# Kernel optimization log

Measured on AMD Instinct MI355X. Metric: run time of the kernel, lower is better.

The kernel has to match this reference:

```python
import jax, jax.numpy as jnp
import numpy as np

TEMPERATURE = 0.1
NEG_INF = -1e30


def setup_inputs() -> dict:
    key = jax.random.key(0)
    kf, kl = jax.random.split(key)
    N, D = 8192, 128
    features = jax.random.normal(kf, (N, D), dtype=jnp.float32)
    # labels in [-1, 80): -1 marks background rows that are filtered out
    labels = jax.random.randint(kl, (N,), -1, 80)
    return {"features": features, "labels": labels}


def reference(features, labels):
    N = labels.shape[0]
    fg = labels >= 0  # [N]

    # F.normalize(p=2, dim=1): x / max(||x||, eps)
    norm = jnp.maximum(jnp.linalg.norm(features, axis=1, keepdims=True), 1e-12)
    f = features / norm

    sim = jnp.matmul(f, f.T) / TEMPERATURE  # [N, N]

    pair_fg = fg[:, None] & fg[None, :]
    eye = jnp.eye(N, dtype=bool)
    label_eq = labels[:, None] == labels[None, :]
    pos_mask = pair_fg & label_eq & ~eye          # positives (same label, not self)
    all_mask = pair_fg & ~eye                     # pos | neg == everything but self (within fg)

    # row-wise masked max, clamped to [-20, 20] as in the original
    max_sim = jnp.max(jnp.where(all_mask, sim, NEG_INF), axis=1)
    max_sim = jnp.clip(max_sim, -20.0, 20.0)

    e = jnp.exp(sim - max_sim[:, None])           # cos-sim/temp is bounded, no overflow
    pos_sum = jnp.clip(jnp.sum(jnp.where(pos_mask, e, 0.0), axis=1), 1e-6, 1e6)
    all_sum = jnp.clip(jnp.sum(jnp.where(all_mask, e, 0.0), axis=1), 1e-6, 1e6)

    loss_i = jnp.minimum(-jnp.log(pos_sum / all_sum), 10.0)  # clamp(max=10)

    # rows contributing to the mean: fg rows with at least one positive
    valid = fg & (jnp.sum(pos_mask, axis=1) > 0)
    n_valid = jnp.sum(valid)
    mean_loss = jnp.sum(jnp.where(valid, loss_i, 0.0)) / jnp.maximum(n_valid, 1).astype(jnp.float32)

    ok = (jnp.sum(fg) >= 2) & (n_valid > 0)
    return jnp.where(ok, mean_loss, jnp.float32(0.0))
```

## Files before the change

kernel.cpp:

```cpp
#include <hip/hip_runtime.h>

#define N 8192
#define D 128
#define CHUNK 512
#define NCHUNK (N / CHUNK)
#define TILE_IT (CHUNK / 128)
#define NBIN 81

typedef unsigned short u16;
typedef __attribute__((ext_vector_type(8))) __bf16 bf16x8;
typedef __attribute__((ext_vector_type(4))) float f32x4;

#define PREP_SCALE 3.7982889979f

__device__ __forceinline__ u16 f2bf(float x) {
  unsigned u = __float_as_uint(x);
  u += 0x7fff + ((u >> 16) & 1);
  return (u16)(u >> 16);
}
__device__ __forceinline__ float bf2f(u16 h) {
  return __uint_as_float(((unsigned)h) << 16);
}

__global__ __launch_bounds__(256) void cpe_sort(const int* __restrict__ labels,
                                                int* __restrict__ perm,
                                                int* __restrict__ slab,
                                                float* __restrict__ acc3) {
  __shared__ int hist[NBIN];
  __shared__ int base[NBIN];
  const int t = threadIdx.x;
  if (t < NBIN) hist[t] = 0;
  if (t < 4) acc3[t] = 0.0f;
  __syncthreads();
  for (int i = t; i < N; i += 256) atomicAdd(&hist[labels[i] + 1], 1);
  __syncthreads();
  if (t == 0) {
    int s = 0;
    for (int b = 0; b < NBIN; ++b) { base[b] = s; s += hist[b]; }
  }
  __syncthreads();
  for (int i = t; i < N; i += 256) {
    const int lab = labels[i];
    const int pos = atomicAdd(&base[lab + 1], 1);
    perm[pos] = i;
    slab[pos] = lab;
  }
}

__global__ __launch_bounds__(256) void cpe_prep(const float* __restrict__ feat,
                                                const int* __restrict__ perm,
                                                u16* __restrict__ fhi,
                                                u16* __restrict__ flo) {
  const int w = threadIdx.x >> 6, l = threadIdx.x & 63;
  const int srow = blockIdx.x * 4 + w;
  const int row = perm[srow];
  const float2 x = *(const float2*)&feat[row * D + l * 2];
  float s = x.x * x.x + x.y * x.y;
#pragma unroll
  for (int sh = 1; sh < 64; sh <<= 1) s += __shfl_xor(s, sh);
  const float inv = PREP_SCALE / fmaxf(sqrtf(s), 1e-12f);
  const float a = x.x * inv, b = x.y * inv;
  const u16 ah = f2bf(a), bh = f2bf(b);
  const u16 al = f2bf(a - bf2f(ah)), bl = f2bf(b - bf2f(bh));
  *(ushort2*)&fhi[srow * D + l * 2] = make_ushort2(ah, bh);
  *(ushort2*)&flo[srow * D + l * 2] = make_ushort2(al, bl);
}

__global__ __launch_bounds__(256, 2) void cpe_main(
    const u16* __restrict__ fhi, const u16* __restrict__ flo,
    const int* __restrict__ slab, float4* __restrict__ partials) {
  __shared__ __align__(16) u16 Bh[128 * 128];
  __shared__ __align__(16) u16 Bl[128 * 128];
  __shared__ int Lab[CHUNK];
  const int rt = blockIdx.x, cc = blockIdx.y;
  const int tid = threadIdx.x;
  const int w = tid >> 6, l = tid & 63, q = l >> 4, m = l & 15;
  const int r0w = rt * 256 + w * 64;
  const int cbase0 = cc * CHUNK;

  Lab[tid] = slab[cbase0 + tid];
  Lab[tid + 256] = slab[cbase0 + 256 + tid];

  const int labi_lo = slab[r0w], labi_hi = slab[r0w + 63];

  bf16x8 Ah[4][4];
  int labi[4][4];
#pragma unroll
  for (int tr = 0; tr < 4; ++tr) {
    const int row = r0w + tr * 16 + m;
#pragma unroll
    for (int ks = 0; ks < 4; ++ks)
      Ah[tr][ks] = *(const bf16x8*)&fhi[row * D + ks * 32 + q * 8];
#pragma unroll
    for (int v = 0; v < 4; ++v) labi[tr][v] = slab[r0w + tr * 16 + q * 4 + v];
  }

  float mxe[4][4], ps[4][4], as_[4][4];
#pragma unroll
  for (int tr = 0; tr < 4; ++tr)
#pragma unroll
    for (int v = 0; v < 4; ++v) { mxe[tr][v] = 0.f; ps[tr][v] = 0.f; as_[tr][v] = 0.f; }

  for (int it = 0; it < TILE_IT; ++it) {
    const int cbase = cbase0 + it * 128;
    __syncthreads();
#pragma unroll
    for (int n = 0; n < 8; ++n) {
      const int r = w * 32 + n * 4 + q;
      const int c = m ^ (r & 15);
      const u16* gh = &fhi[(size_t)(cbase + r) * D + c * 8];
      const u16* gl = &flo[(size_t)(cbase + r) * D + c * 8];
      __builtin_amdgcn_global_load_lds(
          (const __attribute__((address_space(1))) unsigned*)gh,
          (__attribute__((address_space(3))) unsigned*)&Bh[(w * 512 + n * 64) * 8],
          16, 0, 0);
      __builtin_amdgcn_global_load_lds(
          (const __attribute__((address_space(1))) unsigned*)gl,
          (__attribute__((address_space(3))) unsigned*)&Bl[(w * 512 + n * 64) * 8],
          16, 0, 0);
    }
    __syncthreads();

    for (int ct = 0; ct < 8; ++ct) {
      const int tb = it * 128 + ct * 16;
      const int labj_lo = Lab[tb], labj_hi = Lab[tb + 15];
      if (labj_hi < 0) continue;
      const bool slow = (labj_lo < 0) | ((labj_hi >= labi_lo) & (labj_lo <= labi_hi));
      const int jj = ct * 16 + m;
      f32x4 acc[4];
#pragma unroll
      for (int tr = 0; tr < 4; ++tr) acc[tr] = (f32x4){0.f, 0.f, 0.f, 0.f};
#pragma unroll
      for (int ks = 0; ks < 4; ++ks) {
        const int off = jj * 128 + ((ks * 4 + q) ^ m) * 8;
        const bf16x8 bh = *(const bf16x8*)&Bh[off];
        const bf16x8 bl = *(const bf16x8*)&Bl[off];
#pragma unroll
        for (int tr = 0; tr < 4; ++tr)
          acc[tr] = __builtin_amdgcn_mfma_f32_16x16x32_bf16(Ah[tr][ks], bh, acc[tr], 0, 0, 0);
#pragma unroll
        for (int tr = 0; tr < 4; ++tr)
          acc[tr] = __builtin_amdgcn_mfma_f32_16x16x32_bf16(Ah[tr][ks], bl, acc[tr], 0, 0, 0);
      }
      if (!slow) {
#pragma unroll
        for (int tr = 0; tr < 4; ++tr)
#pragma unroll
          for (int v = 0; v < 4; ++v) {
            const float e = __builtin_amdgcn_exp2f(acc[tr][v]);
            as_[tr][v] += e;
            mxe[tr][v] = fmaxf(mxe[tr][v], e);
          }
      } else {
        const int labj = Lab[tb + m];
        const bool fgj = labj >= 0;
        const int jbase = cbase + ct * 16;
#pragma unroll
        for (int tr = 0; tr < 4; ++tr) {
          if (jbase == r0w + tr * 16) {
#pragma unroll
            for (int v = 0; v < 4; ++v) {
              const float e = __builtin_amdgcn_exp2f(acc[tr][v]);
              const float em = (fgj && (m != q * 4 + v)) ? e : 0.0f;
              as_[tr][v] += em;
              mxe[tr][v] = fmaxf(mxe[tr][v], em);
              ps[tr][v] += (labj == labi[tr][v]) ? em : 0.0f;
            }
          } else {
#pragma unroll
            for (int v = 0; v < 4; ++v) {
              const float e = __builtin_amdgcn_exp2f(acc[tr][v]);
              const float em = fgj ? e : 0.0f;
              as_[tr][v] += em;
              mxe[tr][v] = fmaxf(mxe[tr][v], em);
              ps[tr][v] += (labj == labi[tr][v]) ? em : 0.0f;
            }
          }
        }
      }
    }
  }

#pragma unroll
  for (int tr = 0; tr < 4; ++tr)
#pragma unroll
    for (int v = 0; v < 4; ++v) {
      float vm = mxe[tr][v], vp = ps[tr][v], va = as_[tr][v];
#pragma unroll
      for (int s = 1; s < 16; s <<= 1) {
        vm = fmaxf(vm, __shfl_xor(vm, s));
        vp += __shfl_xor(vp, s);
        va += __shfl_xor(va, s);
      }
      if (m == 0)
        partials[(size_t)cc * N + r0w + tr * 16 + q * 4 + v] =
            make_float4(vm, vp, va, 0.f);
    }
}

__global__ __launch_bounds__(256) void cpe_rows(const float4* __restrict__ partials,
                                                const int* __restrict__ slab,
                                                float* __restrict__ acc3,
                                                float* __restrict__ out) {
  const int r = blockIdx.x * 256 + threadIdx.x;
  float mxe = 0.f, ps = 0.f, as_ = 0.f;
#pragma unroll
  for (int c = 0; c < NCHUNK; ++c) {
    const float4 p = partials[(size_t)c * N + r];
    mxe = fmaxf(mxe, p.x); ps += p.y; as_ += p.z;
  }
  const bool fg = slab[r] >= 0;
  const bool valid = fg && (ps > 0.f);
  const float pos = fminf(fmaxf(ps / mxe, 1e-6f), 1e6f);
  const float all = fminf(fmaxf(as_ / mxe, 1e-6f), 1e6f);
  const float loss = fminf(-logf(pos / all), 10.0f);
  float v0 = valid ? loss : 0.f;
  float v1 = valid ? 1.f : 0.f;
  float v2 = fg ? 1.f : 0.f;
#pragma unroll
  for (int s = 1; s < 64; s <<= 1) {
    v0 += __shfl_xor(v0, s); v1 += __shfl_xor(v1, s); v2 += __shfl_xor(v2, s);
  }
  __shared__ float red[3][4];
  const int w = threadIdx.x >> 6, l = threadIdx.x & 63;
  if (l == 0) { red[0][w] = v0; red[1][w] = v1; red[2][w] = v2; }
  __syncthreads();
  if (threadIdx.x == 0) {
    atomicAdd(&acc3[0], red[0][0] + red[0][1] + red[0][2] + red[0][3]);
    atomicAdd(&acc3[1], red[1][0] + red[1][1] + red[1][2] + red[1][3]);
    atomicAdd(&acc3[2], red[2][0] + red[2][1] + red[2][2] + red[2][3]);
    __threadfence();
    const unsigned old = atomicAdd((unsigned*)&acc3[3], 1u);
    if (old == gridDim.x - 1) {
      const float ls = atomicAdd(&acc3[0], 0.0f);
      const float nv = atomicAdd(&acc3[1], 0.0f);
      const float nf = atomicAdd(&acc3[2], 0.0f);
      out[0] = (nf >= 2.0f && nv > 0.0f) ? ls / fmaxf(nv, 1.0f) : 0.0f;
    }
  }
}

extern "C" void kernel_launch(void* const* d_in, const int* in_sizes, int n_in,
                              void* d_out, int out_size, void* d_ws, size_t ws_size,
                              hipStream_t stream) {
  const float* feat = (const float*)d_in[0];
  const int* labels = (const int*)d_in[1];
  float* out = (float*)d_out;
  char* ws = (char*)d_ws;
  u16* fhi = (u16*)ws;
  u16* flo = (u16*)(ws + (size_t)N * D * 2);
  float4* partials = (float4*)(ws + (size_t)N * D * 4);
  float* acc3 = (float*)(ws + (size_t)N * D * 4 + (size_t)NCHUNK * N * 16);
  int* perm = (int*)(ws + (size_t)N * D * 4 + (size_t)NCHUNK * N * 16 + 256);
  int* slab = perm + N;

  cpe_sort<<<1, 256, 0, stream>>>(labels, perm, slab, acc3);
  cpe_prep<<<N / 4, 256, 0, stream>>>(feat, perm, fhi, flo);
  cpe_main<<<dim3(N / 256, NCHUNK), 256, 0, stream>>>(fhi, flo, slab, partials);
  cpe_rows<<<N / 256, 256, 0, stream>>>(partials, slab, acc3, out);
}
```

Baseline: 125.8 us.

## Fuse label sort into prep, drop row-max, fold row reduction into main

```diff
diff --git a/kernel.cpp b/kernel.cpp
--- a/kernel.cpp
+++ b/kernel.cpp
@@ -6,6 +6,7 @@
 #define NCHUNK (N / CHUNK)
 #define TILE_IT (CHUNK / 128)
 #define NBIN 81
+#define NBLK 512
 
 typedef unsigned short u16;
 typedef __attribute__((ext_vector_type(8))) __bf16 bf16x8;
@@ -22,56 +23,75 @@
   return __uint_as_float(((unsigned)h) << 16);
 }
 
-__global__ __launch_bounds__(256) void cpe_sort(const int* __restrict__ labels,
-                                                int* __restrict__ perm,
+__global__ __launch_bounds__(256) void cpe_prep(const float* __restrict__ feat,
+                                                const int* __restrict__ labels,
+                                                u16* __restrict__ fhi,
+                                                u16* __restrict__ flo,
                                                 int* __restrict__ slab,
-                                                float* __restrict__ acc3) {
-  __shared__ int hist[NBIN];
-  __shared__ int base[NBIN];
-  const int t = threadIdx.x;
-  if (t < NBIN) hist[t] = 0;
-  if (t < 4) acc3[t] = 0.0f;
-  __syncthreads();
-  for (int i = t; i < N; i += 256) atomicAdd(&hist[labels[i] + 1], 1);
-  __syncthreads();
-  if (t == 0) {
+                                                float* __restrict__ pacc,
+                                                unsigned* __restrict__ ctr) {
+  __shared__ int hist[4][NBIN], part[4][NBIN], lbase[NBIN], lpos[16];
+  const int tid = threadIdx.x;
+  const int w = tid >> 6, l = tid & 63;
+  const int bid = blockIdx.x;
+  if (tid < NBIN) {
+#pragma unroll
+    for (int cp = 0; cp < 4; ++cp) { hist[cp][tid] = 0; part[cp][tid] = 0; }
+  }
+  if (tid < 32) pacc[bid * 32 + tid] = 0.0f;
+  if (bid == 0 && tid == 0) *ctr = 0u;
+  __syncthreads();
+  const int myBase = bid * 16;
+  for (int j = tid; j < N; j += 256) {
+    const int lab = labels[j] + 1;
+    atomicAdd(&hist[w][lab], 1);
+    if (j < myBase) atomicAdd(&part[w][lab], 1);
+  }
+  __syncthreads();
+  if (tid < NBIN) {
+    hist[0][tid] += hist[1][tid] + hist[2][tid] + hist[3][tid];
+    part[0][tid] += part[1][tid] + part[2][tid] + part[3][tid];
+  }
+  __syncthreads();
+  if (tid == 0) {
     int s = 0;
-    for (int b = 0; b < NBIN; ++b) { base[b] = s; s += hist[b]; }
-  }
-  __syncthreads();
-  for (int i = t; i < N; i += 256) {
-    const int lab = labels[i];
-    const int pos = atomicAdd(&base[lab + 1], 1);
-    perm[pos] = i;
-    slab[pos] = lab;
-  }
-}
-
-__global__ __launch_bounds__(256) void cpe_prep(const float* __restrict__ feat,
-                                                const int* __restrict__ perm,
-                                                u16* __restrict__ fhi,
-                                                u16* __restrict__ flo) {
-  const int w = threadIdx.x >> 6, l = threadIdx.x & 63;
-  const int srow = blockIdx.x * 4 + w;
-  const int row = perm[srow];
-  const float2 x = *(const float2*)&feat[row * D + l * 2];
-  float s = x.x * x.x + x.y * x.y;
-#pragma unroll
-  for (int sh = 1; sh < 64; sh <<= 1) s += __shfl_xor(s, sh);
-  const float inv = PREP_SCALE / fmaxf(sqrtf(s), 1e-12f);
-  const float a = x.x * inv, b = x.y * inv;
-  const u16 ah = f2bf(a), bh = f2bf(b);
-  const u16 al = f2bf(a - bf2f(ah)), bl = f2bf(b - bf2f(bh));
-  *(ushort2*)&fhi[srow * D + l * 2] = make_ushort2(ah, bh);
-  *(ushort2*)&flo[srow * D + l * 2] = make_ushort2(al, bl);
+    for (int b = 0; b < NBIN; ++b) { lbase[b] = s; s += hist[0][b]; }
+  }
+  __syncthreads();
+  if (tid < 16) {
+    const int L = labels[myBase + tid] + 1;
+    int pos = lbase[L] + part[0][L];
+    for (int k = 0; k < tid; ++k) pos += (labels[myBase + k] + 1 == L) ? 1 : 0;
+    lpos[tid] = pos;
+    slab[pos] = L - 1;
+  }
+  __syncthreads();
+#pragma unroll
+  for (int rr = 0; rr < 4; ++rr) {
+    const int k = w * 4 + rr;
+    const float2 x = *(const float2*)&feat[(myBase + k) * D + l * 2];
+    float s = x.x * x.x + x.y * x.y;
+#pragma unroll
+    for (int sh = 1; sh < 64; sh <<= 1) s += __shfl_xor(s, sh);
+    const float inv = PREP_SCALE / fmaxf(sqrtf(s), 1e-12f);
+    const float a = x.x * inv, b = x.y * inv;
+    const u16 ah = f2bf(a), bh = f2bf(b);
+    const u16 al = f2bf(a - bf2f(ah)), bl = f2bf(b - bf2f(bh));
+    const int pos = lpos[k];
+    *(ushort2*)&fhi[pos * D + l * 2] = make_ushort2(ah, bh);
+    *(ushort2*)&flo[pos * D + l * 2] = make_ushort2(al, bl);
+  }
 }
 
 __global__ __launch_bounds__(256, 2) void cpe_main(
     const u16* __restrict__ fhi, const u16* __restrict__ flo,
-    const int* __restrict__ slab, float4* __restrict__ partials) {
+    const int* __restrict__ slab, float* __restrict__ pacc,
+    unsigned* __restrict__ ctr, float* __restrict__ out) {
   __shared__ __align__(16) u16 Bh[128 * 128];
   __shared__ __align__(16) u16 Bl[128 * 128];
   __shared__ int Lab[CHUNK];
+  __shared__ float red[3][4];
+  __shared__ int isLast;
   const int rt = blockIdx.x, cc = blockIdx.y;
   const int tid = threadIdx.x;
   const int w = tid >> 6, l = tid & 63, q = l >> 4, m = l & 15;
@@ -95,11 +115,11 @@
     for (int v = 0; v < 4; ++v) labi[tr][v] = slab[r0w + tr * 16 + q * 4 + v];
   }
 
-  float mxe[4][4], ps[4][4], as_[4][4];
+  float ps[4][4], as_[4][4];
 #pragma unroll
   for (int tr = 0; tr < 4; ++tr)
 #pragma unroll
-    for (int v = 0; v < 4; ++v) { mxe[tr][v] = 0.f; ps[tr][v] = 0.f; as_[tr][v] = 0.f; }
+    for (int v = 0; v < 4; ++v) { ps[tr][v] = 0.f; as_[tr][v] = 0.f; }
 
   for (int it = 0; it < TILE_IT; ++it) {
     const int cbase = cbase0 + it * 128;
@@ -146,11 +166,8 @@
 #pragma unroll
         for (int tr = 0; tr < 4; ++tr)
 #pragma unroll
-          for (int v = 0; v < 4; ++v) {
-            const float e = __builtin_amdgcn_exp2f(acc[tr][v]);
-            as_[tr][v] += e;
-            mxe[tr][v] = fmaxf(mxe[tr][v], e);
-          }
+          for (int v = 0; v < 4; ++v)
+            as_[tr][v] += __builtin_amdgcn_exp2f(acc[tr][v]);
       } else {
         const int labj = Lab[tb + m];
         const bool fgj = labj >= 0;
@@ -163,7 +180,6 @@
               const float e = __builtin_amdgcn_exp2f(acc[tr][v]);
               const float em = (fgj && (m != q * 4 + v)) ? e : 0.0f;
               as_[tr][v] += em;
-              mxe[tr][v] = fmaxf(mxe[tr][v], em);
               ps[tr][v] += (labj == labi[tr][v]) ? em : 0.0f;
             }
           } else {
@@ -172,7 +188,6 @@
               const float e = __builtin_amdgcn_exp2f(acc[tr][v]);
               const float em = fgj ? e : 0.0f;
               as_[tr][v] += em;
-              mxe[tr][v] = fmaxf(mxe[tr][v], em);
               ps[tr][v] += (labj == labi[tr][v]) ? em : 0.0f;
             }
           }
@@ -185,56 +200,51 @@
   for (int tr = 0; tr < 4; ++tr)
 #pragma unroll
     for (int v = 0; v < 4; ++v) {
-      float vm = mxe[tr][v], vp = ps[tr][v], va = as_[tr][v];
+      float vp = ps[tr][v], va = as_[tr][v];
 #pragma unroll
       for (int s = 1; s < 16; s <<= 1) {
-        vm = fmaxf(vm, __shfl_xor(vm, s));
         vp += __shfl_xor(vp, s);
         va += __shfl_xor(va, s);
       }
-      if (m == 0)
-        partials[(size_t)cc * N + r0w + tr * 16 + q * 4 + v] =
-            make_float4(vm, vp, va, 0.f);
-    }
-}
-
-__global__ __launch_bounds__(256) void cpe_rows(const float4* __restrict__ partials,
-                                                const int* __restrict__ slab,
-                                                float* __restrict__ acc3,
-                                                float* __restrict__ out) {
-  const int r = blockIdx.x * 256 + threadIdx.x;
-  float mxe = 0.f, ps = 0.f, as_ = 0.f;
-#pragma unroll
-  for (int c = 0; c < NCHUNK; ++c) {
-    const float4 p = partials[(size_t)c * N + r];
-    mxe = fmaxf(mxe, p.x); ps += p.y; as_ += p.z;
-  }
-  const bool fg = slab[r] >= 0;
-  const bool valid = fg && (ps > 0.f);
-  const float pos = fminf(fmaxf(ps / mxe, 1e-6f), 1e6f);
-  const float all = fminf(fmaxf(as_ / mxe, 1e-6f), 1e6f);
-  const float loss = fminf(-logf(pos / all), 10.0f);
-  float v0 = valid ? loss : 0.f;
-  float v1 = valid ? 1.f : 0.f;
-  float v2 = fg ? 1.f : 0.f;
-#pragma unroll
-  for (int s = 1; s < 64; s <<= 1) {
-    v0 += __shfl_xor(v0, s); v1 += __shfl_xor(v1, s); v2 += __shfl_xor(v2, s);
-  }
-  __shared__ float red[3][4];
-  const int w = threadIdx.x >> 6, l = threadIdx.x & 63;
-  if (l == 0) { red[0][w] = v0; red[1][w] = v1; red[2][w] = v2; }
-  __syncthreads();
-  if (threadIdx.x == 0) {
-    atomicAdd(&acc3[0], red[0][0] + red[0][1] + red[0][2] + red[0][3]);
-    atomicAdd(&acc3[1], red[1][0] + red[1][1] + red[1][2] + red[1][3]);
-    atomicAdd(&acc3[2], red[2][0] + red[2][1] + red[2][2] + red[2][3]);
+      if (m == 0) {
+        const int r = r0w + tr * 16 + q * 4 + v;
+        atomicAdd(&pacc[2 * r], vp);
+        atomicAdd(&pacc[2 * r + 1], va);
+      }
+    }
+
+  __syncthreads();
+  if (tid == 0) {
     __threadfence();
-    const unsigned old = atomicAdd((unsigned*)&acc3[3], 1u);
-    if (old == gridDim.x - 1) {
-      const float ls = atomicAdd(&acc3[0], 0.0f);
-      const float nv = atomicAdd(&acc3[1], 0.0f);
-      const float nf = atomicAdd(&acc3[2], 0.0f);
+    isLast = (atomicAdd(ctr, 1u) == NBLK - 1) ? 1 : 0;
+  }
+  __syncthreads();
+  if (isLast) {
+    float v0 = 0.f, v1 = 0.f, v2 = 0.f;
+#pragma unroll 4
+    for (int k = 0; k < 32; ++k) {
+      const int r = k * 256 + tid;
+      const float psr = atomicAdd(&pacc[2 * r], 0.0f);
+      const float asr = atomicAdd(&pacc[2 * r + 1], 0.0f);
+      const bool fg = slab[r] >= 0;
+      const bool valid = fg && (psr > 0.f);
+      const float loss = fminf(logf(asr / psr), 10.0f);
+      v0 += valid ? loss : 0.f;
+      v1 += valid ? 1.f : 0.f;
+      v2 += fg ? 1.f : 0.f;
+    }
+#pragma unroll
+    for (int s = 1; s < 64; s <<= 1) {
+      v0 += __shfl_xor(v0, s);
+      v1 += __shfl_xor(v1, s);
+      v2 += __shfl_xor(v2, s);
+    }
+    if (l == 0) { red[0][w] = v0; red[1][w] = v1; red[2][w] = v2; }
+    __syncthreads();
+    if (tid == 0) {
+      const float ls = red[0][0] + red[0][1] + red[0][2] + red[0][3];
+      const float nv = red[1][0] + red[1][1] + red[1][2] + red[1][3];
+      const float nf = red[2][0] + red[2][1] + red[2][2] + red[2][3];
       out[0] = (nf >= 2.0f && nv > 0.0f) ? ls / fmaxf(nv, 1.0f) : 0.0f;
     }
   }
@@ -249,13 +259,10 @@
   char* ws = (char*)d_ws;
   u16* fhi = (u16*)ws;
   u16* flo = (u16*)(ws + (size_t)N * D * 2);
-  float4* partials = (float4*)(ws + (size_t)N * D * 4);
-  float* acc3 = (float*)(ws + (size_t)N * D * 4 + (size_t)NCHUNK * N * 16);
-  int* perm = (int*)(ws + (size_t)N * D * 4 + (size_t)NCHUNK * N * 16 + 256);
-  int* slab = perm + N;
-
-  cpe_sort<<<1, 256, 0, stream>>>(labels, perm, slab, acc3);
-  cpe_prep<<<N / 4, 256, 0, stream>>>(feat, perm, fhi, flo);
-  cpe_main<<<dim3(N / 256, NCHUNK), 256, 0, stream>>>(fhi, flo, slab, partials);
-  cpe_rows<<<N / 256, 256, 0, stream>>>(partials, slab, acc3, out);
-}
+  float* pacc = (float*)(ws + (size_t)N * D * 4);
+  int* slab = (int*)(ws + (size_t)N * D * 4 + (size_t)N * 8);
+  unsigned* ctr = (unsigned*)(ws + (size_t)N * D * 4 + (size_t)N * 8 + (size_t)N * 4);
+
+  cpe_prep<<<NBLK, 256, 0, stream>>>(feat, labels, fhi, flo, slab, pacc, ctr);
+  cpe_main<<<dim3(N / 256, NCHUNK), 256, 0, stream>>>(fhi, flo, slab, pacc, ctr, out);
+}
```

Measured after the change: 121.7 us. -3.3%, faster.
